# Kernel tuning notes

Measured on AMD Instinct MI355X. Metric: run time of the kernel, lower is better.

## Reference

```python
import jax, jax.numpy as jnp
import numpy as np

B, T, V = 2, 2048, 256
C, H, L = 1024, 16, 8
DH = C // H  # 64


def setup_inputs() -> dict:
    key = jax.random.key(0)
    ks = jax.random.split(key, 12)
    s = 0.02
    return {
        "x": jax.random.normal(ks[0], (B, T, V), jnp.float32),
        "W_emb": jax.random.normal(ks[1], (V, C), jnp.float32) * s,
        "b_emb": jnp.zeros((C,), jnp.float32),
        "pos": jax.random.normal(ks[2], (1, T, C), jnp.float32) * s,
        "Wqkv": jax.random.normal(ks[3], (L, C, 3 * C), jnp.float32) * s,
        "bqkv": jnp.zeros((L, 3 * C), jnp.float32),
        "Wproj": jax.random.normal(ks[4], (L, C, C), jnp.float32) * s,
        "bproj": jnp.zeros((L, C), jnp.float32),
        "gamma": jnp.ones((C,), jnp.float32),
        "beta": jnp.zeros((C,), jnp.float32),
        "W_out": jax.random.normal(ks[5], (C, V), jnp.float32) * s,
        "b_out": jnp.zeros((V,), jnp.float32),
    }


def _attn_block(h, Wqkv_l, bqkv_l, Wproj_l, bproj_l):
    # h: [B, T, C]
    qkv = h @ Wqkv_l + bqkv_l                      # [B, T, 3C]
    q, k, v = jnp.split(qkv, 3, axis=-1)
    q = q.reshape(B, T, H, DH)
    k = k.reshape(B, T, H, DH)
    v = v.reshape(B, T, H, DH)
    scale = 1.0 / np.sqrt(DH).astype(np.float32)
    att = jnp.einsum("bthd,bshd->bhts", q, k) * scale   # [B, H, T, T]
    att = jax.nn.softmax(att, axis=-1)
    y = jnp.einsum("bhts,bshd->bthd", att, v)            # [B, T, H, DH]
    y = y.reshape(B, T, C)
    return y @ Wproj_l + bproj_l


def reference(x, W_emb, b_emb, pos, Wqkv, bqkv, Wproj, bproj, gamma, beta, W_out, b_out):
    h = x @ W_emb + b_emb            # dense embedding: Linear(V -> C)
    h = h + pos[:, :T, :]
    # NOTE: original blocks return attention output directly (no residual, no MLP)
    def body(h, params):
        Wq, bq, Wp, bp = params
        return _attn_block(h, Wq, bq, Wp, bp), None
    h, _ = jax.lax.scan(body, h, (Wqkv, bqkv, Wproj, bproj))
    # LayerNorm
    mu = jnp.mean(h, axis=-1, keepdims=True)
    var = jnp.mean(jnp.square(h - mu), axis=-1, keepdims=True)
    h = (h - mu) * jax.lax.rsqrt(var + 1e-5) * gamma + beta
    return h @ W_out + b_out          # [B, T, V]
```

## Files before the change

kernel.cpp:

```cpp
#include <hip/hip_runtime.h>
#include <hip/hip_bf16.h>

#define T_SEQ 2048
#define BATCH 2
#define CDIM 1024
#define VDIM 256
#define NHEAD 16
#define DHEAD 64
#define NLAYER 8
#define MROWS (BATCH * T_SEQ)

typedef __attribute__((ext_vector_type(8))) short bf16x8;
typedef __attribute__((ext_vector_type(4))) float f32x4;
typedef __attribute__((ext_vector_type(4))) int i32x4;

#define SELHI 0x07060302u
#define SELLO 0x05040100u
#define QSCALE 0.18033688011112042f

__device__ __forceinline__ uint prm(uint a, uint b, uint s) { return __builtin_amdgcn_perm(a, b, s); }

__device__ __forceinline__ uint bf16rne(float f) {
    uint u = __float_as_uint(f);
    return (u + 0x7fffu + ((u >> 16) & 1u)) & 0xffff0000u;
}
__device__ __forceinline__ uint packsplit(float x) {
    uint hb = bf16rne(x);
    float d = x - __uint_as_float(hb);
    uint lb = bf16rne(d);
    return prm(hb, lb, SELHI);
}
__device__ __forceinline__ float unpack2(uint u) {
    return __uint_as_float(u & 0xffff0000u) + __uint_as_float(u << 16);
}
__device__ __forceinline__ bf16x8 asb(i32x4 v) {
    union { i32x4 i; bf16x8 b; } u; u.i = v; return u.b;
}
__device__ __forceinline__ short bfs(float f) { return (short)(bf16rne(f) >> 16); }
__device__ __forceinline__ void gload_lds16(const void* g, void* l) {
    __builtin_amdgcn_global_load_lds(
        (const __attribute__((address_space(1))) void*)g,
        (__attribute__((address_space(3))) void*)l, 16, 0, 0);
}


__global__ __launch_bounds__(256) void packx_kernel(
    const float* __restrict__ x, uint* __restrict__ xpf)
{
    const int t  = blockIdx.x * 256 + threadIdx.x;
    const int m  = t >> 6;
    const int k0 = (t & 63) * 4;
    const float4 v = *(const float4*)&x[(size_t)m * 256 + k0];
    const size_t addr = ((size_t)(m >> 4) * 8 + (k0 >> 5)) * 512
                      + (size_t)(((k0 >> 2) & 3) * 16 + (m & 15)) * 8
                      + 4 * ((k0 >> 4) & 1);
    uint4 pk;
    pk.x = packsplit(v.x); pk.y = packsplit(v.y);
    pk.z = packsplit(v.z); pk.w = packsplit(v.w);
    *(uint4*)&xpf[addr] = pk;
}

__device__ __forceinline__ void wsplit_body(
    const float* __restrict__ W, short* __restrict__ Fh, short* __restrict__ Fl,
    int N, int K, int n, int kq)
{
    const int k0 = kq * 4;
    float f0 = W[(size_t)(k0 + 0) * N + n];
    float f1 = W[(size_t)(k0 + 1) * N + n];
    float f2 = W[(size_t)(k0 + 2) * N + n];
    float f3 = W[(size_t)(k0 + 3) * N + n];
    uint h0 = bf16rne(f0), h1 = bf16rne(f1), h2 = bf16rne(f2), h3 = bf16rne(f3);

    const int gl = kq & 3, j0 = ((kq >> 2) & 1) * 4;
    const size_t base = (((size_t)(n >> 4) * (K >> 5) + (kq >> 3)) * 64 + gl * 16 + (n & 15)) * 8 + j0;
    *(int2*)&Fh[base] = make_int2((int)prm(h1, h0, SELHI), (int)prm(h3, h2, SELHI));
    if (Fl) {
        uint l0 = bf16rne(f0 - __uint_as_float(h0));
        uint l1 = bf16rne(f1 - __uint_as_float(h1));
        uint l2 = bf16rne(f2 - __uint_as_float(h2));
        uint l3 = bf16rne(f3 - __uint_as_float(h3));
        *(int2*)&Fl[base] = make_int2((int)prm(l1, l0, SELHI), (int)prm(l3, l2, SELHI));
    }
}

__global__ __launch_bounds__(256) void wsplit_kernel(
    const float* __restrict__ W, short* __restrict__ Fh, short* __restrict__ Fl,
    int N, int K)
{
    const int ln = threadIdx.x & 63, lk = threadIdx.x >> 6;
    wsplit_body(W, Fh, Fl, N, K, blockIdx.x * 64 + ln, blockIdx.y * 4 + lk);
}

__global__ __launch_bounds__(256) void wsplit2_kernel(
    const float* __restrict__ Wq, short* __restrict__ Fqh,
    const float* __restrict__ Wp, short* __restrict__ Fph, short* __restrict__ Fpl)
{
    const int ln = threadIdx.x & 63, lk = threadIdx.x >> 6;
    const int kq = blockIdx.y * 4 + lk;
    if (blockIdx.x < 48)
        wsplit_body(Wq, Fqh, nullptr, 3 * CDIM, CDIM, blockIdx.x * 64 + ln, kq);
    else
        wsplit_body(Wp, Fph, Fpl, CDIM, CDIM, (blockIdx.x - 48) * 64 + ln, kq);
}

__global__ __launch_bounds__(256) void gemm_lds1_kernel(
    const short* __restrict__ Ahf, const short* __restrict__ Bhf,
    const float* __restrict__ bias,
    uint* __restrict__ Cq, short* __restrict__ Ckf, short* __restrict__ Cvf,
    int M, int N, int K)
{
    __shared__ __align__(16) short Asm[8][2][64][8];
    __shared__ __align__(16) short Bsm[8][2][64][8];

    const int tid = threadIdx.x, lane = tid & 63, w = tid >> 6;
    const int wr = w >> 1, wc = w & 1, x = lane & 15, gl = lane >> 4;
    const int bm = blockIdx.y * 128, bn = blockIdx.x * 128;
    const int nkc = K >> 5;
    const int nks = K >> 6;
    const size_t tstr = (size_t)nkc * 512;

    const short* sbase = (w < 2)
        ? Ahf + ((size_t)((bm >> 4) + 4 * w) * nkc) * 512 + (size_t)lane * 8
        : Bhf + ((size_t)((bn >> 4) + 4 * (w - 2)) * nkc) * 512 + (size_t)lane * 8;
    short* dbase = (w < 2) ? &Asm[4 * w][0][0][0] : &Bsm[4 * (w - 2)][0][0][0];

    f32x4 acc[4][4];
#pragma unroll
    for (int mi = 0; mi < 4; ++mi)
#pragma unroll
        for (int ni = 0; ni < 4; ++ni) acc[mi][ni] = (f32x4){0.f, 0.f, 0.f, 0.f};

    for (int kk = 0; kk < nks; ++kk) {
        __syncthreads();
#pragma unroll
        for (int i = 0; i < 4; ++i)
#pragma unroll
            for (int ch = 0; ch < 2; ++ch)
                gload_lds16(sbase + i * tstr + (size_t)(2 * kk + ch) * 512,
                            dbase + (i * 2 + ch) * 512);
        __syncthreads();

        bf16x8 ah[4][2], bh[4][2];
#pragma unroll
        for (int t = 0; t < 4; ++t)
#pragma unroll
            for (int ch = 0; ch < 2; ++ch) {
                ah[t][ch] = *(const bf16x8*)&Asm[wr * 4 + t][ch][lane][0];
                bh[t][ch] = *(const bf16x8*)&Bsm[wc * 4 + t][ch][lane][0];
            }
        __builtin_amdgcn_s_setprio(1);
#pragma unroll
        for (int mi = 0; mi < 4; ++mi)
#pragma unroll
            for (int ni = 0; ni < 4; ++ni) {
                acc[mi][ni] = __builtin_amdgcn_mfma_f32_16x16x32_bf16(ah[mi][0], bh[ni][0], acc[mi][ni], 0, 0, 0);
                acc[mi][ni] = __builtin_amdgcn_mfma_f32_16x16x32_bf16(ah[mi][1], bh[ni][1], acc[mi][ni], 0, 0, 0);
            }
        __builtin_amdgcn_s_setprio(0);
    }

#pragma unroll
    for (int ni = 0; ni < 4; ++ni) {
        const int n = bn + wc * 64 + ni * 16 + x;
        const float bv = bias[n];
#pragma unroll
        for (int mi = 0; mi < 4; ++mi) {
            const int m0 = bm + wr * 64 + mi * 16 + gl * 4;
            const f32x4 o = acc[mi][ni];
            if (n < 1024) {
                Cq[(size_t)(m0 + 0) * 1024 + n] = packsplit((o[0] + bv) * QSCALE);
                Cq[(size_t)(m0 + 1) * 1024 + n] = packsplit((o[1] + bv) * QSCALE);
                Cq[(size_t)(m0 + 2) * 1024 + n] = packsplit((o[2] + bv) * QSCALE);
                Cq[(size_t)(m0 + 3) * 1024 + n] = packsplit((o[3] + bv) * QSCALE);
            } else if (n < 2048) {
                const int dd6 = n - 1024;
                const int hhh = dd6 >> 6, ch = (dd6 >> 5) & 1, dd = dd6 & 31;
                const int bq = m0 >> 11, sv = m0 & (T_SEQ - 1);
                const size_t base = ((((size_t)(bq * NHEAD + hhh) * 128 + (sv >> 4)) * 2 + ch) * 64
                                    + 16 * ((dd & 15) >> 2) + (sv & 15)) * 8
                                    + (dd & 3) + 4 * (dd >> 4);
                Ckf[base + 0]  = bfs(o[0] + bv);
                Ckf[base + 8]  = bfs(o[1] + bv);
                Ckf[base + 16] = bfs(o[2] + bv);
                Ckf[base + 24] = bfs(o[3] + bv);
            } else {
                const int dd6 = n - 2048;
                const int hhh = dd6 >> 6, dmi = (dd6 >> 4) & 3, xt = dd6 & 15;
                const int bq = m0 >> 11, sv = m0 & (T_SEQ - 1);
                const size_t base = ((((size_t)(bq * NHEAD + hhh) * 64 + (sv >> 5)) * 4 + dmi) * 64
                                    + xt + 16 * ((sv & 15) >> 2)) * 8 + 4 * ((sv >> 4) & 1);
                short4 st;
                st.x = bfs(o[0] + bv); st.y = bfs(o[1] + bv);
                st.z = bfs(o[2] + bv); st.w = bfs(o[3] + bv);
                *(short4*)&Cvf[base] = st;
            }
        }
    }
}

template <int TERMS, int NI>
__global__ __launch_bounds__(256) void gemm_mfma_kernel(
    const uint* __restrict__ Apf, const short* __restrict__ Ahf,
    const short* __restrict__ Bhf, const short* __restrict__ Blf,
    const float* __restrict__ bias, const float* __restrict__ addrow,
    uint* __restrict__ Cv, short* __restrict__ Chf,
    int M, int N, int K, int out_mode)
{
    const int tid = threadIdx.x, lane = tid & 63, w = tid >> 6;
    const int wr = w >> 1, wc = w & 1, x = lane & 15, gl = lane >> 4;
    const int bm = blockIdx.y * 128, bn = blockIdx.x * (32 * NI);
    const int nkc = K >> 5;

    const uint*  ab  = Apf ? Apf + ((size_t)((bm >> 4) + wr * 4) * nkc) * 512 + (size_t)lane * 8 : nullptr;
    const short* abh = Ahf ? Ahf + (((size_t)((bm >> 4) + wr * 4) * nkc) * 64 + lane) * 8 : nullptr;
    const short* hb  = Bhf + (((size_t)((bn >> 4) + wc * NI) * nkc) * 64 + lane) * 8;
    const short* lb  = Blf + (((size_t)((bn >> 4) + wc * NI) * nkc) * 64 + lane) * 8;
    const size_t tstrA = (size_t)nkc * 512;
    const size_t tstrF = (size_t)nkc * 512;

    f32x4 acc[4][NI];
#pragma unroll
    for (int mi = 0; mi < 4; ++mi)
#pragma unroll
        for (int ni = 0; ni < NI; ++ni) acc[mi][ni] = (f32x4){0.f, 0.f, 0.f, 0.f};

    for (int kc = 0; kc < nkc; ++kc) {
        const size_t ko = (size_t)kc * 512;
        bf16x8 ah[4], al[4], bh[NI], bl[NI];
#pragma unroll
        for (int t = 0; t < 4; ++t) {
            if (TERMS == 1) {
                ah[t] = *(const bf16x8*)(abh + t * tstrF + ko);
            } else {
                const uint* ap = ab + t * tstrA + ko;
                uint4 a0 = *(const uint4*)ap;
                uint4 a1 = *(const uint4*)(ap + 4);
                i32x4 h4, l4;
                h4[0] = (int)prm(a0.y, a0.x, SELHI); h4[1] = (int)prm(a0.w, a0.z, SELHI);
                h4[2] = (int)prm(a1.y, a1.x, SELHI); h4[3] = (int)prm(a1.w, a1.z, SELHI);
                l4[0] = (int)prm(a0.y, a0.x, SELLO); l4[1] = (int)prm(a0.w, a0.z, SELLO);
                l4[2] = (int)prm(a1.y, a1.x, SELLO); l4[3] = (int)prm(a1.w, a1.z, SELLO);
                ah[t] = asb(h4); al[t] = asb(l4);
            }
        }
#pragma unroll
        for (int t = 0; t < NI; ++t) {
            bh[t] = *(const bf16x8*)(hb + t * tstrF + ko);
            if (TERMS >= 3) bl[t] = *(const bf16x8*)(lb + t * tstrF + ko);
        }
        __builtin_amdgcn_s_setprio(1);
#pragma unroll
        for (int mi = 0; mi < 4; ++mi)
#pragma unroll
            for (int ni = 0; ni < NI; ++ni) {
                acc[mi][ni] = __builtin_amdgcn_mfma_f32_16x16x32_bf16(ah[mi], bh[ni], acc[mi][ni], 0, 0, 0);
                if (TERMS >= 3)
                    acc[mi][ni] = __builtin_amdgcn_mfma_f32_16x16x32_bf16(ah[mi], bl[ni], acc[mi][ni], 0, 0, 0);
                if (TERMS >= 2)
                    acc[mi][ni] = __builtin_amdgcn_mfma_f32_16x16x32_bf16(al[mi], bh[ni], acc[mi][ni], 0, 0, 0);
            }
        __builtin_amdgcn_s_setprio(0);
    }

#pragma unroll
    for (int ni = 0; ni < NI; ++ni) {
        const int n = bn + wc * (16 * NI) + ni * 16 + x;
        const float bv = bias[n];
#pragma unroll
        for (int mi = 0; mi < 4; ++mi) {
            const int m0 = bm + wr * 64 + mi * 16 + gl * 4;
            const f32x4 o = acc[mi][ni];
            if (out_mode == 0) {
                float* C = (float*)Cv;
                C[(size_t)(m0 + 0) * N + n] = o[0] + bv;
                C[(size_t)(m0 + 1) * N + n] = o[1] + bv;
                C[(size_t)(m0 + 2) * N + n] = o[2] + bv;
                C[(size_t)(m0 + 3) * N + n] = o[3] + bv;
            } else {
                float p0 = 0.f, p1 = 0.f, p2 = 0.f, p3 = 0.f;
                if (addrow) {
                    p0 = addrow[(size_t)((m0 + 0) & (T_SEQ - 1)) * N + n];
                    p1 = addrow[(size_t)((m0 + 1) & (T_SEQ - 1)) * N + n];
                    p2 = addrow[(size_t)((m0 + 2) & (T_SEQ - 1)) * N + n];
                    p3 = addrow[(size_t)((m0 + 3) & (T_SEQ - 1)) * N + n];
                }
                const float v0 = o[0] + bv + p0, v1 = o[1] + bv + p1;
                const float v2 = o[2] + bv + p2, v3 = o[3] + bv + p3;
                const size_t mt = (size_t)(bm >> 4) + wr * 4 + mi;
                const size_t base = (mt * (N >> 5) + (n >> 5)) * 512
                                  + (size_t)(((n >> 2) & 3) * 16 + gl * 4) * 8
                                  + (n & 3) + 4 * ((n >> 4) & 1);
                Cv[base + 0 * 8] = packsplit(v0);
                Cv[base + 1 * 8] = packsplit(v1);
                Cv[base + 2 * 8] = packsplit(v2);
                Cv[base + 3 * 8] = packsplit(v3);
                if (Chf) {
                    const size_t fb = ((mt * (N >> 5) + (n >> 5)) * 64
                                      + ((n >> 2) & 3) * 16 + gl * 4) * 8
                                      + (n & 3) + 4 * ((n >> 4) & 1);
                    Chf[fb + 0 * 8] = bfs(v0);
                    Chf[fb + 1 * 8] = bfs(v1);
                    Chf[fb + 2 * 8] = bfs(v2);
                    Chf[fb + 3 * 8] = bfs(v3);
                }
            }
        }
    }
}

__global__ __launch_bounds__(256) void attn_mfma_kernel(
    const uint* __restrict__ qrow, const short* __restrict__ kf,
    const short* __restrict__ vf, uint* __restrict__ y)
{
    const int tid  = threadIdx.x;
    const int w    = tid >> 6;
    const int lane = tid & 63;
    const int x    = lane & 15;
    const int gl   = lane >> 4;

    const int orig = blockIdx.x;
    const int wgid = (orig & 7) * 64 + (orig >> 3);
    const int bh = wgid >> 4;
    const int b = bh >> 4, hh = bh & 15;
    const int t0 = (wgid & 15) * 128;

    i32x4 qhi[2][2];
#pragma unroll
    for (int qf = 0; qf < 2; ++qf) {
        const uint* qp = qrow + (size_t)(b * T_SEQ + t0 + 64 * qf + 16 * w + x) * 1024 + hh * 64;
#pragma unroll
        for (int ch = 0; ch < 2; ++ch) {
            uint4 a0 = *(const uint4*)(qp + 32 * ch + 4 * gl);
            uint4 a1 = *(const uint4*)(qp + 32 * ch + 16 + 4 * gl);
            qhi[qf][ch][0] = (int)prm(a0.y, a0.x, SELHI); qhi[qf][ch][1] = (int)prm(a0.w, a0.z, SELHI);
            qhi[qf][ch][2] = (int)prm(a1.y, a1.x, SELHI); qhi[qf][ch][3] = (int)prm(a1.w, a1.z, SELHI);
        }
    }

    const short* kb = kf + (size_t)bh * 128 * 2 * 512 + (size_t)lane * 8;
    const short* vb = vf + (size_t)bh * 64 * 4 * 512 + (size_t)lane * 8;

    i32x4 ones4;
    ones4[0] = ones4[1] = ones4[2] = ones4[3] = 0x3F803F80;

    f32x4 oacc[2][4], lacc[2];
#pragma unroll
    for (int qf = 0; qf < 2; ++qf) {
        lacc[qf] = (f32x4){0.f, 0.f, 0.f, 0.f};
#pragma unroll
        for (int i = 0; i < 4; ++i) oacc[qf][i] = (f32x4){0.f, 0.f, 0.f, 0.f};
    }

    for (int s0 = 0; s0 < T_SEQ; s0 += 64) {
        bf16x8 kh[4][2], vh[2][4];
#pragma unroll
        for (int sc = 0; sc < 4; ++sc)
#pragma unroll
            for (int ch = 0; ch < 2; ++ch)
                kh[sc][ch] = *(const bf16x8*)(kb + ((((size_t)(s0 >> 4) + sc) * 2 + ch) * 512));
#pragma unroll
        for (int ch = 0; ch < 2; ++ch)
#pragma unroll
            for (int dm = 0; dm < 4; ++dm)
                vh[ch][dm] = *(const bf16x8*)(vb + ((((size_t)(s0 >> 5) + ch) * 4 + dm) * 512));

#pragma unroll
        for (int qf = 0; qf < 2; ++qf) {
            f32x4 s4[4];
#pragma unroll
            for (int sc = 0; sc < 4; ++sc) {
                s4[sc] = (f32x4){0.f, 0.f, 0.f, 0.f};
                s4[sc] = __builtin_amdgcn_mfma_f32_16x16x32_bf16(kh[sc][0], asb(qhi[qf][0]), s4[sc], 0, 0, 0);
                s4[sc] = __builtin_amdgcn_mfma_f32_16x16x32_bf16(kh[sc][1], asb(qhi[qf][1]), s4[sc], 0, 0, 0);
            }
#pragma unroll
            for (int sc = 0; sc < 4; ++sc) {
                s4[sc][0] = __builtin_amdgcn_exp2f(s4[sc][0]);
                s4[sc][1] = __builtin_amdgcn_exp2f(s4[sc][1]);
                s4[sc][2] = __builtin_amdgcn_exp2f(s4[sc][2]);
                s4[sc][3] = __builtin_amdgcn_exp2f(s4[sc][3]);
            }
            i32x4 pfh[2];
#pragma unroll
            for (int c = 0; c < 2; ++c) {
                f32x4 pa = s4[2 * c], pb = s4[2 * c + 1];
                pfh[c][0] = (int)prm(__float_as_uint(pa[1]), __float_as_uint(pa[0]), SELHI);
                pfh[c][1] = (int)prm(__float_as_uint(pa[3]), __float_as_uint(pa[2]), SELHI);
                pfh[c][2] = (int)prm(__float_as_uint(pb[1]), __float_as_uint(pb[0]), SELHI);
                pfh[c][3] = (int)prm(__float_as_uint(pb[3]), __float_as_uint(pb[2]), SELHI);
            }
            lacc[qf] = __builtin_amdgcn_mfma_f32_16x16x32_bf16(asb(ones4), asb(pfh[0]), lacc[qf], 0, 0, 0);
            lacc[qf] = __builtin_amdgcn_mfma_f32_16x16x32_bf16(asb(ones4), asb(pfh[1]), lacc[qf], 0, 0, 0);
#pragma unroll
            for (int dm = 0; dm < 4; ++dm) {
                oacc[qf][dm] = __builtin_amdgcn_mfma_f32_16x16x32_bf16(vh[0][dm], asb(pfh[0]), oacc[qf][dm], 0, 0, 0);
                oacc[qf][dm] = __builtin_amdgcn_mfma_f32_16x16x32_bf16(vh[1][dm], asb(pfh[1]), oacc[qf][dm], 0, 0, 0);
            }
        }
    }

#pragma unroll
    for (int qf = 0; qf < 2; ++qf) {
        const float invl = 1.f / lacc[qf][0];
        const size_t mt = (size_t)((b * T_SEQ + t0) >> 4) + 4 * qf + w;
#pragma unroll
        for (int dm = 0; dm < 4; ++dm) {
            f32x4 o = oacc[qf][dm];
            const size_t addr = (mt * 32 + hh * 2 + (dm >> 1)) * 512
                              + (size_t)lane * 8 + 4 * (dm & 1);
            uint4 pk;
            pk.x = packsplit(o[0] * invl); pk.y = packsplit(o[1] * invl);
            pk.z = packsplit(o[2] * invl); pk.w = packsplit(o[3] * invl);
            *(uint4*)&y[addr] = pk;
        }
    }
}

__global__ __launch_bounds__(256) void ln_kernel(
    const uint* __restrict__ h, const float* __restrict__ gamma,
    const float* __restrict__ beta, uint* __restrict__ outp)
{
    const int row = blockIdx.x;
    const int tid = threadIdx.x;

    const size_t addr = ((size_t)(row >> 4) * 32 + (tid >> 3)) * 512
                      + (size_t)((tid & 3) * 16 + (row & 15)) * 8
                      + 4 * ((tid >> 2) & 1);
    uint4 u = *(const uint4*)&h[addr];
    float4 v;
    v.x = unpack2(u.x); v.y = unpack2(u.y); v.z = unpack2(u.z); v.w = unpack2(u.w);

    float s  = v.x + v.y + v.z + v.w;
    float ss = v.x * v.x + v.y * v.y + v.z * v.z + v.w * v.w;
#pragma unroll
    for (int off = 1; off < 64; off <<= 1) {
        s  += __shfl_xor(s, off);
        ss += __shfl_xor(ss, off);
    }
    __shared__ float rs[4], rss[4];
    const int wid = tid >> 6;
    if ((tid & 63) == 0) { rs[wid] = s; rss[wid] = ss; }
    __syncthreads();
    s  = rs[0] + rs[1] + rs[2] + rs[3];
    ss = rss[0] + rss[1] + rss[2] + rss[3];

    const float mu   = s * (1.f / (float)CDIM);
    const float var  = ss * (1.f / (float)CDIM) - mu * mu;
    const float rstd = rsqrtf(var + 1e-5f);

    const float4 g  = *(const float4*)&gamma[tid * 4];
    const float4 be = *(const float4*)&beta[tid * 4];
    uint4 pk;
    pk.x = packsplit((v.x - mu) * rstd * g.x + be.x);
    pk.y = packsplit((v.y - mu) * rstd * g.y + be.y);
    pk.z = packsplit((v.z - mu) * rstd * g.z + be.z);
    pk.w = packsplit((v.w - mu) * rstd * g.w + be.w);
    *(uint4*)&outp[addr] = pk;
}

extern "C" void kernel_launch(void* const* d_in, const int* in_sizes, int n_in,
                              void* d_out, int out_size, void* d_ws, size_t ws_size,
                              hipStream_t stream)
{
    const float* x      = (const float*)d_in[0];
    const float* W_emb  = (const float*)d_in[1];
    const float* b_emb  = (const float*)d_in[2];
    const float* pos    = (const float*)d_in[3];
    const float* Wqkv   = (const float*)d_in[4];
    const float* bqkv   = (const float*)d_in[5];
    const float* Wproj  = (const float*)d_in[6];
    const float* bproj  = (const float*)d_in[7];
    const float* gamma  = (const float*)d_in[8];
    const float* beta   = (const float*)d_in[9];
    const float* W_out  = (const float*)d_in[10];
    const float* b_out  = (const float*)d_in[11];
    float* out = (float*)d_out;

    uint* h    = (uint*)d_ws;
    uint* qrow = h + (size_t)MROWS * CDIM;
    uint* y    = qrow + (size_t)MROWS * CDIM;
    short* kf  = (short*)(y + (size_t)MROWS * CDIM);
    short* vfb = kf + (size_t)32 * 128 * 2 * 512;
    short* hf  = vfb + (size_t)32 * 64 * 4 * 512;
    short* Bqh = hf + (size_t)MROWS * CDIM;
    short* Bph = Bqh + (size_t)3 * CDIM * CDIM;
    short* Bpl = Bph + (size_t)CDIM * CDIM;
    short* Eh  = Bpl + (size_t)CDIM * CDIM;
    short* El  = Eh  + (size_t)VDIM * CDIM;
    short* Oh  = El  + (size_t)VDIM * CDIM;
    short* Ol  = Oh  + (size_t)CDIM * VDIM;
    uint*  xpf = (uint*)(Ol + (size_t)CDIM * VDIM);

    const dim3 blk(256);
    const int nattn = (T_SEQ / 128) * BATCH * NHEAD;

    packx_kernel<<<dim3(MROWS * (VDIM / 4) / 256), blk, 0, stream>>>(x, xpf);
    wsplit_kernel<<<dim3(CDIM / 64, VDIM / 16), blk, 0, stream>>>(W_emb, Eh, El, CDIM, VDIM);
    gemm_mfma_kernel<3, 4><<<dim3(CDIM / 128, MROWS / 128), blk, 0, stream>>>(
        xpf, nullptr, Eh, El, b_emb, pos, h, hf, MROWS, CDIM, VDIM, 2);

    for (int l = 0; l < NLAYER; ++l) {
        wsplit2_kernel<<<dim3(64, CDIM / 16), blk, 0, stream>>>(
            Wqkv + (size_t)l * CDIM * 3 * CDIM, Bqh,
            Wproj + (size_t)l * CDIM * CDIM, Bph, Bpl);
        gemm_lds1_kernel<<<dim3(3 * CDIM / 128, MROWS / 128), blk, 0, stream>>>(
            hf, Bqh, bqkv + (size_t)l * 3 * CDIM, qrow, kf, vfb, MROWS, 3 * CDIM, CDIM);
        attn_mfma_kernel<<<dim3(nattn), blk, 0, stream>>>(qrow, kf, vfb, y);
        gemm_mfma_kernel<3, 2><<<dim3(CDIM / 64, MROWS / 128), blk, 0, stream>>>(
            y, nullptr, Bph, Bpl, bproj + (size_t)l * CDIM, nullptr,
            h, hf, MROWS, CDIM, CDIM, 2);
    }

    ln_kernel<<<dim3(MROWS), blk, 0, stream>>>(h, gamma, beta, qrow);
    wsplit_kernel<<<dim3(VDIM / 64, CDIM / 16), blk, 0, stream>>>(W_out, Oh, Ol, VDIM, CDIM);
    gemm_mfma_kernel<3, 1><<<dim3(VDIM / 32, MROWS / 128), blk, 0, stream>>>(
        qrow, nullptr, Oh, Ol, b_out, nullptr, (uint*)out, nullptr, MROWS, VDIM, CDIM, 0);
}
```

Measured before the change: 1.023 ms.

## Double-buffer LDS tiles in QKV GEMM to overlap loads with MFMA

```diff
diff --git a/kernel.cpp b/kernel.cpp
--- a/kernel.cpp
+++ b/kernel.cpp
@@ -109,20 +109,20 @@
     uint* __restrict__ Cq, short* __restrict__ Ckf, short* __restrict__ Cvf,
     int M, int N, int K)
 {
-    __shared__ __align__(16) short Asm[8][2][64][8];
-    __shared__ __align__(16) short Bsm[8][2][64][8];
+    __shared__ __align__(16) short Asm[2][8][64][8];
+    __shared__ __align__(16) short Bsm[2][8][64][8];
 
     const int tid = threadIdx.x, lane = tid & 63, w = tid >> 6;
     const int wr = w >> 1, wc = w & 1, x = lane & 15, gl = lane >> 4;
     const int bm = blockIdx.y * 128, bn = blockIdx.x * 128;
     const int nkc = K >> 5;
-    const int nks = K >> 6;
     const size_t tstr = (size_t)nkc * 512;
 
     const short* sbase = (w < 2)
         ? Ahf + ((size_t)((bm >> 4) + 4 * w) * nkc) * 512 + (size_t)lane * 8
         : Bhf + ((size_t)((bn >> 4) + 4 * (w - 2)) * nkc) * 512 + (size_t)lane * 8;
-    short* dbase = (w < 2) ? &Asm[4 * w][0][0][0] : &Bsm[4 * (w - 2)][0][0][0];
+    short* d0 = (w < 2) ? &Asm[0][4 * w][0][0] : &Bsm[0][4 * (w - 2)][0][0];
+    short* d1 = (w < 2) ? &Asm[1][4 * w][0][0] : &Bsm[1][4 * (w - 2)][0][0];
 
     f32x4 acc[4][4];
 #pragma unroll
@@ -130,33 +130,33 @@
 #pragma unroll
         for (int ni = 0; ni < 4; ++ni) acc[mi][ni] = (f32x4){0.f, 0.f, 0.f, 0.f};
 
-    for (int kk = 0; kk < nks; ++kk) {
+#pragma unroll
+    for (int i = 0; i < 4; ++i)
+        gload_lds16(sbase + i * tstr, d0 + i * 512);
+    __syncthreads();
+
+    for (int kc = 0; kc < nkc; ++kc) {
+        const int cur = kc & 1;
+        if (kc + 1 < nkc) {
+            short* nxt = cur ? d0 : d1;
+#pragma unroll
+            for (int i = 0; i < 4; ++i)
+                gload_lds16(sbase + i * tstr + (size_t)(kc + 1) * 512, nxt + i * 512);
+        }
+        bf16x8 ah[4], bh[4];
+#pragma unroll
+        for (int t = 0; t < 4; ++t) {
+            ah[t] = *(const bf16x8*)&Asm[cur][wr * 4 + t][lane][0];
+            bh[t] = *(const bf16x8*)&Bsm[cur][wc * 4 + t][lane][0];
+        }
+        __builtin_amdgcn_s_setprio(1);
+#pragma unroll
+        for (int mi = 0; mi < 4; ++mi)
+#pragma unroll
+            for (int ni = 0; ni < 4; ++ni)
+                acc[mi][ni] = __builtin_amdgcn_mfma_f32_16x16x32_bf16(ah[mi], bh[ni], acc[mi][ni], 0, 0, 0);
+        __builtin_amdgcn_s_setprio(0);
         __syncthreads();
-#pragma unroll
-        for (int i = 0; i < 4; ++i)
-#pragma unroll
-            for (int ch = 0; ch < 2; ++ch)
-                gload_lds16(sbase + i * tstr + (size_t)(2 * kk + ch) * 512,
-                            dbase + (i * 2 + ch) * 512);
-        __syncthreads();
-
-        bf16x8 ah[4][2], bh[4][2];
-#pragma unroll
-        for (int t = 0; t < 4; ++t)
-#pragma unroll
-            for (int ch = 0; ch < 2; ++ch) {
-                ah[t][ch] = *(const bf16x8*)&Asm[wr * 4 + t][ch][lane][0];
-                bh[t][ch] = *(const bf16x8*)&Bsm[wc * 4 + t][ch][lane][0];
-            }
-        __builtin_amdgcn_s_setprio(1);
-#pragma unroll
-        for (int mi = 0; mi < 4; ++mi)
-#pragma unroll
-            for (int ni = 0; ni < 4; ++ni) {
-                acc[mi][ni] = __builtin_amdgcn_mfma_f32_16x16x32_bf16(ah[mi][0], bh[ni][0], acc[mi][ni], 0, 0, 0);
-                acc[mi][ni] = __builtin_amdgcn_mfma_f32_16x16x32_bf16(ah[mi][1], bh[ni][1], acc[mi][ni], 0, 0, 0);
-            }
-        __builtin_amdgcn_s_setprio(0);
     }
 
 #pragma unroll
```

Result: no change. 1.029 ms (+0.6%).
